# Kernel optimization log

Measured on AMD Instinct MI355X. Metric: run time of the kernel, lower is better.

## Reference

```python
import jax, jax.numpy as jnp
import numpy as np

B, L, G, N, K, E = 64, 512, 128, 32, 8, 65536
NTOK, D_TOK, H_DIR, NTL_INP, NHID, NREL = 10000, 64, 64, 32, 16, 16


def _bn(x, gamma, beta, eps=1e-5):
    # training-mode BatchNorm1d over axis 0; x: (n, C)
    mu = x.mean(0)
    var = x.var(0)
    return gamma * (x - mu) / jnp.sqrt(var + eps) + beta


def _lstm(x, w_ih, w_hh, b_ih, b_hh):
    # x: (B, T, D); torch gate order i, f, g, o
    nb = x.shape[0]
    H = w_hh.shape[1]
    def step(carry, xt):
        h, c = carry
        g = xt @ w_ih.T + b_ih + h @ w_hh.T + b_hh
        i, f, gg, o = jnp.split(g, 4, axis=-1)
        c = jax.nn.sigmoid(f) * c + jax.nn.sigmoid(i) * jnp.tanh(gg)
        h = jax.nn.sigmoid(o) * jnp.tanh(c)
        return (h, c), h
    init = (jnp.zeros((nb, H), x.dtype), jnp.zeros((nb, H), x.dtype))
    _, hs = jax.lax.scan(step, init, jnp.swapaxes(x, 0, 1))
    return jnp.swapaxes(hs, 0, 1)


def setup_inputs() -> dict:
    key = jax.random.key(0)
    ks = jax.random.split(key, 24)
    inp = {}
    inp['seq'] = jax.random.randint(ks[0], (B, L), 0, NTOK)
    inp['pos2grp'] = jax.random.randint(ks[1], (B, L), 0, G)
    inp['idx'] = jax.random.randint(ks[2], (B, N, K), 0, L)
    inp['u'] = jax.random.randint(ks[3], (E,), 0, B * N)
    inp['v'] = jax.random.randint(ks[4], (E,), 0, B * N)
    # parameters
    s = 1.0 / np.sqrt(H_DIR)
    inp['tok_emb'] = jax.random.normal(ks[5], (NTOK, D_TOK), jnp.float32)
    for tag, k0 in (('f', 6), ('b', 10)):
        inp[f'w_ih_{tag}'] = s * jax.random.normal(ks[k0], (4 * H_DIR, D_TOK), jnp.float32)
        inp[f'w_hh_{tag}'] = s * jax.random.normal(ks[k0 + 1], (4 * H_DIR, H_DIR), jnp.float32)
        inp[f'b_ih_{tag}'] = s * jax.random.normal(ks[k0 + 2], (4 * H_DIR,), jnp.float32)
        inp[f'b_hh_{tag}'] = s * jax.random.normal(ks[k0 + 3], (4 * H_DIR,), jnp.float32)
    inp['w_src'] = (1.0 / np.sqrt(2 * H_DIR)) * jax.random.normal(ks[14], (NTL_INP, 2 * H_DIR), jnp.float32)
    inp['b_src'] = jnp.zeros((NTL_INP,), jnp.float32)
    inp['w_dst'] = (1.0 / np.sqrt(2 * H_DIR)) * jax.random.normal(ks[15], (NTL_INP, 2 * H_DIR), jnp.float32)
    inp['b_dst'] = jnp.zeros((NTL_INP,), jnp.float32)
    inp['g_src'] = jnp.ones((NTL_INP,), jnp.float32)
    inp['be_src'] = jnp.zeros((NTL_INP,), jnp.float32)
    inp['g_dst'] = jnp.ones((NTL_INP,), jnp.float32)
    inp['be_dst'] = jnp.zeros((NTL_INP,), jnp.float32)
    inp['ntl_w'] = 0.001 * jax.random.normal(ks[16], (NREL, NHID, NTL_INP, NTL_INP), jnp.float32)
    inp['ntl_v'] = 0.001 * jax.random.normal(ks[17], (NREL, NHID, 2 * NTL_INP), jnp.float32)
    inp['ntl_b'] = jnp.zeros((NREL, NHID, 1), jnp.float32)
    inp['ntl_u'] = 0.001 * jax.random.normal(ks[18], (NREL, 1, NHID), jnp.float32)
    inp['ntl_g'] = jnp.ones((NREL * NHID,), jnp.float32)
    inp['ntl_be'] = jnp.zeros((NREL * NHID,), jnp.float32)
    return inp


def reference(seq, pos2grp, idx, u, v, tok_emb,
              w_ih_f, w_hh_f, b_ih_f, b_hh_f,
              w_ih_b, w_hh_b, b_ih_b, b_hh_b,
              w_src, b_src, w_dst, b_dst,
              g_src, be_src, g_dst, be_dst,
              ntl_w, ntl_v, ntl_b, ntl_u, ntl_g, ntl_be):
    # token embed + scatter-sum tokens -> groups
    x_tok = tok_emb[seq]                                   # (B, L, D)
    gid = (pos2grp + jnp.arange(B)[:, None] * G).reshape(-1)
    x_grp = jax.ops.segment_sum(x_tok.reshape(B * L, -1), gid,
                                num_segments=B * G).reshape(B, G, -1)
    # bidirectional LSTM over groups
    hf = _lstm(x_grp, w_ih_f, w_hh_f, b_ih_f, b_hh_f)
    hb = jnp.flip(_lstm(jnp.flip(x_grp, 1), w_ih_b, w_hh_b, b_ih_b, b_hh_b), 1)
    h_grp = jnp.concatenate([hf, hb], -1)                  # (B, G, 2H)
    # hierarchical gather + sum: node <- sum over K token positions' groups
    b_idx = jnp.arange(B)[:, None, None]
    g_idx = pos2grp[b_idx, idx]                            # (B, N, K)
    h = h_grp[b_idx, g_idx].sum(2).reshape(B * N, -1)      # (B*N, 2H)
    # edge endpoint projections + batchnorm
    hs = _bn(h[u] @ w_src.T + b_src, g_src, be_src)        # (E, ninp)
    ht = _bn(h[v] @ w_dst.T + b_dst, g_dst, be_dst)
    # Neural Tensor Layer
    linear = jnp.einsum('rhd,nd->rhn', ntl_v, jnp.concatenate([hs, ht], 1))
    bil = jnp.stack([
        jnp.einsum('nhj,nj->hn', jnp.einsum('ni,hij->nhj', hs, ntl_w[r]), ht)
        for r in range(NREL)], 0)                          # (R, H, E)
    z = bil + linear + ntl_b
    mu = z.mean(-1, keepdims=True)
    var = z.var(-1, keepdims=True)
    zn = ntl_g.reshape(NREL, NHID, 1) * (z - mu) / jnp.sqrt(var + 1e-5) \
         + ntl_be.reshape(NREL, NHID, 1)
    t = jnp.tanh(zn)
    logit = jnp.einsum('rh,rhn->nr', ntl_u[:, 0, :], t)    # (E, R)
    return logit
```

## Files before the change

kernel.cpp:

```cpp
#include <hip/hip_runtime.h>
#include <hip/hip_bf16.h>
#include <hip/hip_fp16.h>
#include <cstdint>

constexpr int B_   = 64;
constexpr int L_   = 512;
constexpr int G_   = 128;
constexpr int E_   = 65536;
constexpr int RH   = 256;
constexpr int M_   = 2048;
constexpr int JA   = 33;
constexpr int COLS = RH * JA;
constexpr int NREP = 16;

typedef _Float16 v2h __attribute__((ext_vector_type(2)));
typedef _Float16 v8h __attribute__((ext_vector_type(8)));
typedef float    v4f __attribute__((ext_vector_type(4)));
typedef union { uint4 u4; v8h h8; } cvt8;

#define DEV static __device__ __forceinline__

DEV float sigm(float x) { return 1.f / (1.f + __expf(-x)); }
DEV float tanh_fast(float x) {
    x = fminf(15.f, fmaxf(-15.f, x));
    float e = __expf(2.f * x);
    return (e - 1.f) / (e + 1.f);
}

__global__ __launch_bounds__(256) void k_eh(const int* __restrict__ seq,
                                            const int* __restrict__ p2g,
                                            const float* __restrict__ emb,
                                            const int* __restrict__ u,
                                            const int* __restrict__ v,
                                            const float* __restrict__ ntlw,
                                            const float* __restrict__ ntlv,
                                            const float* __restrict__ ntlb,
                                            float* __restrict__ xg,
                                            int* __restrict__ cu, int* __restrict__ cv,
                                            float* __restrict__ waug) {
    int blk = blockIdx.x;
    int t   = threadIdx.x;
    if (blk >= 320) {
        int gid = (blk - 320) * 256 + t;
        int i   = gid / COLS;
        int rem = gid - i * COLS;
        int rh  = rem / JA;
        int j   = rem - rh * JA;
        float val;
        if (i < 32) val = (j < 32) ? ntlw[((size_t)rh * 32 + i) * 32 + j] : ntlv[rh * 64 + i];
        else        val = (j < 32) ? ntlv[rh * 64 + 32 + j] : ntlb[rh];
        waug[(size_t)i * COLS + j * 256 + rh] = val;
        return;
    }
    if (blk >= 64) {
        int n = (blk - 64) * 256 + t;
        atomicAdd(&cu[u[n]], 1);
        atomicAdd(&cv[v[n]], 1);
        return;
    }
    __shared__ float xgl[G_ * 64];
    for (int i = t; i < G_ * 64; i += 256) xgl[i] = 0.f;
    __syncthreads();
    int b = blk;
    int d = t & 63, part = t >> 6;
#pragma unroll 8
    for (int l = part; l < L_; l += 4) {
        int s = seq[b * L_ + l];
        int g = p2g[b * L_ + l];
        atomicAdd(&xgl[g * 64 + d], emb[s * 64 + d]);
    }
    __syncthreads();
    for (int i = t; i < G_ * 64; i += 256) xg[(size_t)b * G_ * 64 + i] = xgl[i];
}

__global__ __launch_bounds__(256) void k_pre(const float* __restrict__ xg,
                                             const float* __restrict__ wihf,
                                             const float* __restrict__ bihf,
                                             const float* __restrict__ bhhf,
                                             const float* __restrict__ wihb,
                                             const float* __restrict__ bihb,
                                             const float* __restrict__ bhhb,
                                             float* __restrict__ pre,
                                             const int* __restrict__ cu,
                                             int* __restrict__ ustart,
                                             int* __restrict__ ucursor) {
    int blk = blockIdx.x;
    int t   = threadIdx.x;
    if (blk == 512) {
        __shared__ int ps[256];
        int base = t * 8, run = 0;
        int c[8], loc[8];
#pragma unroll
        for (int i = 0; i < 8; i++) c[i] = cu[base + i];
#pragma unroll
        for (int i = 0; i < 8; i++) { loc[i] = run; run += c[i]; }
        ps[t] = run;
        __syncthreads();
        for (int off = 1; off < 256; off <<= 1) {
            int a = (t >= off) ? ps[t - off] : 0;
            __syncthreads();
            ps[t] += a;
            __syncthreads();
        }
        int ex = ps[t] - run;
#pragma unroll
        for (int i = 0; i < 8; i++) { ustart[base + i] = ex + loc[i]; ucursor[base + i] = ex + loc[i]; }
        if (t == 255) ustart[2048] = E_;
        return;
    }
    int dir = blk >> 8;
    const float* wih = dir ? wihb : wihf;
    float bias = dir ? (bihb[t] + bhhb[t]) : (bihf[t] + bhhf[t]);
    int r0 = (blk & 255) * 32;

    float4 wv[16];
#pragma unroll
    for (int c = 0; c < 16; c++) wv[c] = ((const float4*)(wih + t * 64))[c];

#pragma unroll 2
    for (int ml = 0; ml < 32; ml++) {
        const float* xr = xg + (size_t)(r0 + ml) * 64;
        float acc = bias;
#pragma unroll
        for (int c = 0; c < 16; c++) {
            float x0 = xr[4 * c], x1 = xr[4 * c + 1], x2 = xr[4 * c + 2], x3 = xr[4 * c + 3];
            acc += x0 * wv[c].x + x1 * wv[c].y + x2 * wv[c].z + x3 * wv[c].w;
        }
        pre[((size_t)dir * 8192 + r0 + ml) * 256 + t] = acc;
    }
}

template <int HALF>
__global__ __launch_bounds__(256, 1) void k_lstm_h(const float* __restrict__ pre,
                                                   const float* __restrict__ whh_f,
                                                   const float* __restrict__ whh_b,
                                                   float* __restrict__ hgrp,
                                                   float* __restrict__ hstate,
                                                   float* __restrict__ cstate,
                                                   const int* __restrict__ u,
                                                   const int* __restrict__ v,
                                                   int* __restrict__ ucursor,
                                                   int2* __restrict__ eonv) {
    int blk = blockIdx.x;
    int t   = threadIdx.x;
    if (HALF == 0 && blk >= 128) {
        int n = (blk - 128) * 256 + t;
        int pos = atomicAdd(&ucursor[u[n]], 1);
        eonv[pos] = make_int2(n, v[n]);
        return;
    }
    __shared__ __align__(16) float plds[64][256];
    __shared__ __align__(16) float hist[64][64];
    __shared__ float gl[2][256];
    int dir = blk >> 6;
    int b   = blk & 63;
    const float* whh = dir ? whh_b : whh_f;
    const float* src = pre + ((size_t)dir * 8192 + (size_t)b * G_) * 256;
    int e = t & 63;
    int q = t >> 6;

    float4 wv[16];
#pragma unroll
    for (int c = 0; c < 16; c++) wv[c] = ((const float4*)(whh + (size_t)t * 64))[c];

    float h, creg;
    if (HALF == 0) { h = 0.f; creg = 0.f; }
    else           { h = hstate[blk * 64 + e]; creg = cstate[blk * 64 + e]; }

    {
        int base = (dir ^ HALF) ? 64 : 0;
        const float4* s4 = (const float4*)(src + (size_t)base * 256);
        float4* d4 = (float4*)&plds[0][0];
#pragma unroll
        for (int i = 0; i < 16; i++) d4[i * 256 + t] = s4[i * 256 + t];
    }
    __syncthreads();
    for (int kk = 0; kk < 64; kk++) {
        int srow = dir ? (63 - kk) : kk;
        float p = plds[srow][t];
        float a0 = p, a1 = 0.f, a2 = 0.f, a3 = 0.f;
#pragma unroll
        for (int c = 0; c < 16; c++) {
            float f0 = __int_as_float(__builtin_amdgcn_readlane(__float_as_int(h), 4 * c + 0));
            float f1 = __int_as_float(__builtin_amdgcn_readlane(__float_as_int(h), 4 * c + 1));
            float f2 = __int_as_float(__builtin_amdgcn_readlane(__float_as_int(h), 4 * c + 2));
            float f3 = __int_as_float(__builtin_amdgcn_readlane(__float_as_int(h), 4 * c + 3));
            a0 += wv[c].x * f0;
            a1 += wv[c].y * f1;
            a2 += wv[c].z * f2;
            a3 += wv[c].w * f3;
        }
        float g = (a0 + a1) + (a2 + a3);
        gl[kk & 1][t] = (q == 2) ? tanh_fast(g) : sigm(g);
        __syncthreads();
        float ai = gl[kk & 1][e];
        float af = gl[kk & 1][64 + e];
        float ag = gl[kk & 1][128 + e];
        float ao = gl[kk & 1][192 + e];
        creg = af * creg + ai * ag;
        h = ao * tanh_fast(creg);
        if (q == 0) hist[srow][e] = h;
    }
    __syncthreads();
    int sbase = (dir ? (1 - HALF) : HALF) * 64;
#pragma unroll
    for (int i = 0; i < 16; i++) {
        int row = q * 16 + i;
        int s = sbase + row;
        hgrp[((size_t)(b * G_ + s)) * 128 + dir * 64 + e] = hist[row][e];
    }
    if (HALF == 0 && q == 0) {
        hstate[blk * 64 + e] = h;
        cstate[blk * 64 + e] = creg;
    }
}

__global__ __launch_bounds__(256) void k_gp(const int* __restrict__ idx,
                                            const int* __restrict__ p2g,
                                            const float* __restrict__ hgrp,
                                            const int* __restrict__ cu,
                                            const int* __restrict__ cv,
                                            const float* __restrict__ wsrc,
                                            const float* __restrict__ bsrc,
                                            const float* __restrict__ wdst,
                                            const float* __restrict__ bdst,
                                            float* __restrict__ Ps, float* __restrict__ Pd,
                                            float* __restrict__ bn_raw) {
    __shared__ __align__(16) float hsl[8][128];
    __shared__ float red[256];
    int m0 = blockIdx.x * 8;
    int t  = threadIdx.x;
    int d = t & 127, mh = t >> 7;
#pragma unroll
    for (int rep = 0; rep < 4; rep++) {
        int ml = rep * 2 + mh;
        int m  = m0 + ml;
        int b  = m >> 5;
        float acc = 0.f;
#pragma unroll
        for (int k = 0; k < 8; k++) {
            int l = idx[m * 8 + k];
            int g = p2g[b * L_ + l];
            acc += hgrp[((size_t)b * G_ + g) * 128 + d];
        }
        hsl[ml][d] = acc;
    }
    __syncthreads();
    int ml = t >> 5, o = t & 31;
    int m  = m0 + ml;
    const float4* hp = (const float4*)&hsl[ml][0];
    float cw_u = (float)cu[m], cw_v = (float)cv[m];
#pragma unroll 1
    for (int side = 0; side < 2; side++) {
        const float* W = side ? wdst : wsrc;
        float4 wr[32];
#pragma unroll
        for (int c = 0; c < 32; c++) wr[c] = ((const float4*)(W + (size_t)o * 128))[c];
        float acc = side ? bdst[o] : bsrc[o];
#pragma unroll
        for (int c = 0; c < 32; c++) {
            float4 h4 = hp[c];
            acc += h4.x * wr[c].x + h4.y * wr[c].y + h4.z * wr[c].z + h4.w * wr[c].w;
        }
        (side ? Pd : Ps)[(size_t)m * 32 + o] = acc;
        float cw = side ? cw_v : cw_u;
        red[t] = cw * acc;
        __syncthreads();
        if (t < 32) {
            float s = 0.f;
#pragma unroll
            for (int i = 0; i < 8; i++) s += red[i * 32 + t];
            atomicAdd(&bn_raw[side * 64 + t], s);
        }
        __syncthreads();
        red[t] = cw * acc * acc;
        __syncthreads();
        if (t < 32) {
            float s = 0.f;
#pragma unroll
            for (int i = 0; i < 8; i++) s += red[i * 32 + t];
            atomicAdd(&bn_raw[side * 64 + 32 + t], s);
        }
        __syncthreads();
    }
}

__global__ __launch_bounds__(256) void k_prep(const float* __restrict__ Ps,
                                              const float* __restrict__ Pd,
                                              const float* __restrict__ bn_raw,
                                              const float* __restrict__ gs,
                                              const float* __restrict__ bes,
                                              const float* __restrict__ gd,
                                              const float* __restrict__ bed,
                                              float* __restrict__ hsaugT,
                                              v2h* __restrict__ htp) {
    int blk = blockIdx.x;
    int t   = threadIdx.x;
    constexpr float invE = 1.f / (float)E_;
    if (blk < 264) {
        int gid = blk * 256 + t;
        int c = gid >> 11;
        int m = gid & 2047;
        float val = 1.f;
        if (c < 32) {
            float mu  = bn_raw[c] * invE;
            float isd = rsqrtf(bn_raw[32 + c] * invE - mu * mu + 1e-5f);
            val = gs[c] * (Ps[(size_t)m * 32 + c] - mu) * isd + bes[c];
        }
        hsaugT[(size_t)c * 2048 + m] = val;
        return;
    }
    int gid = (blk - 264) * 256 + t;
    int m  = gid >> 4;
    int jp = gid & 15;
    int j0 = 2 * jp, j1 = 2 * jp + 1;
    float mu0  = bn_raw[64 + j0] * invE;
    float isd0 = rsqrtf(bn_raw[96 + j0] * invE - mu0 * mu0 + 1e-5f);
    float mu1  = bn_raw[64 + j1] * invE;
    float isd1 = rsqrtf(bn_raw[96 + j1] * invE - mu1 * mu1 + 1e-5f);
    float h0 = gd[j0] * (Pd[(size_t)m * 32 + j0] - mu0) * isd0 + bed[j0];
    float h1 = gd[j1] * (Pd[(size_t)m * 32 + j1] - mu1) * isd1 + bed[j1];
    v2h p;
    p.x = (_Float16)h0; p.y = (_Float16)h1;
    htp[gid] = p;
}

__global__ __launch_bounds__(256) void k_agemm(const float* __restrict__ hsaugT,
                                               const float* __restrict__ waug,
                                               v2h* __restrict__ Ah,
                                               float* __restrict__ A32) {
    int mt = blockIdx.x;
    int jp = blockIdx.y;
    int t  = threadIdx.x;
    if (jp < 16) {
        float w0[JA], w1[JA];
#pragma unroll
        for (int i = 0; i < JA; i++) {
            w0[i] = waug[(size_t)i * COLS + (2 * jp) * 256 + t];
            w1[i] = waug[(size_t)i * COLS + (2 * jp + 1) * 256 + t];
        }
        float acc0[32], acc1[32];
#pragma unroll
        for (int ml = 0; ml < 32; ml++) { acc0[ml] = 0.f; acc1[ml] = 0.f; }
#pragma unroll 3
        for (int i = 0; i < JA; i++) {
            const float* hr = hsaugT + (size_t)i * 2048 + mt * 32;
#pragma unroll
            for (int ml = 0; ml < 32; ml++) {
                acc0[ml] += hr[ml] * w0[i];
                acc1[ml] += hr[ml] * w1[i];
            }
        }
#pragma unroll
        for (int ml = 0; ml < 32; ml++) {
            v2h p;
            p.x = (_Float16)acc0[ml]; p.y = (_Float16)acc1[ml];
            Ah[(size_t)(mt * 32 + ml) * 4096 + jp * 256 + t] = p;
        }
    } else {
        float w2[JA];
#pragma unroll
        for (int i = 0; i < JA; i++) w2[i] = waug[(size_t)i * COLS + 32 * 256 + t];
        float acc[32];
#pragma unroll
        for (int ml = 0; ml < 32; ml++) acc[ml] = 0.f;
#pragma unroll 3
        for (int i = 0; i < JA; i++) {
            const float* hr = hsaugT + (size_t)i * 2048 + mt * 32;
#pragma unroll
            for (int ml = 0; ml < 32; ml++) acc[ml] += hr[ml] * w2[i];
        }
#pragma unroll
        for (int ml = 0; ml < 32; ml++)
            A32[(size_t)(mt * 32 + ml) * 256 + t] = acc[ml];
    }
}

__global__ __launch_bounds__(256) void k_z(const unsigned int* __restrict__ Ah,
                                           const float* __restrict__ A32,
                                           const uint4* __restrict__ htp4,
                                           const int* __restrict__ ustart,
                                           const int2* __restrict__ eonv,
                                           _Float16* __restrict__ zh,
                                           float* __restrict__ zsumR,
                                           float* __restrict__ zsqR) {
    int t    = threadIdx.x;
    int lane = t & 63;
    int uu   = blockIdx.x * 4 + (t >> 6);
    int l15  = lane & 15, quad = lane >> 4;

    uint4 bf[16];
#pragma unroll
    for (int nt = 0; nt < 16; nt++) {
        const unsigned int* bp = Ah + (size_t)uu * 4096 + (quad * 4) * 256 + nt * 16 + l15;
        bf[nt].x = bp[0]; bf[nt].y = bp[256]; bf[nt].z = bp[512]; bf[nt].w = bp[768];
    }
    float a32[16];
#pragma unroll
    for (int nt = 0; nt < 16; nt++) a32[nt] = A32[(size_t)uu * 256 + nt * 16 + l15];

    float s1[16], s2[16];
#pragma unroll
    for (int nt = 0; nt < 16; nt++) { s1[nt] = 0.f; s2[nt] = 0.f; }

    int e0 = ustart[uu], e1 = ustart[uu + 1];
    for (int base = e0; base < e1; base += 16) {
        int ei = min(base + l15, e1 - 1);
        int2 q = eonv[ei];
        uint4 afu = htp4[(size_t)q.y * 4 + quad];
        cvt8 ac; ac.u4 = afu;
        int nrow[4], valid[4];
#pragma unroll
        for (int r = 0; r < 4; r++) {
            int er = quad * 4 + r;
            nrow[r]  = __builtin_amdgcn_ds_bpermute(er << 2, q.x);
            valid[r] = (base + er) < e1;
        }
#pragma unroll
        for (int nt = 0; nt < 16; nt++) {
            cvt8 bc; bc.u4 = bf[nt];
            v4f acc = { a32[nt], a32[nt], a32[nt], a32[nt] };
            acc = __builtin_amdgcn_mfma_f32_16x16x32_f16(ac.h8, bc.h8, acc, 0, 0, 0);
#pragma unroll
            for (int r = 0; r < 4; r++) {
                if (valid[r]) {
                    float z = acc[r];
                    zh[(size_t)nrow[r] * 256 + nt * 16 + l15] = (_Float16)z;
                    s1[nt] += z; s2[nt] += z * z;
                }
            }
        }
    }
    int rep = (blockIdx.x & (NREP - 1)) * 256;
#pragma unroll
    for (int nt = 0; nt < 16; nt++) {
        float a = s1[nt], b = s2[nt];
        a += __shfl_xor(a, 16); a += __shfl_xor(a, 32);
        b += __shfl_xor(b, 16); b += __shfl_xor(b, 32);
        if (quad == 0) {
            atomicAdd(&zsumR[rep + nt * 16 + l15], a);
            atomicAdd(&zsqR[rep + nt * 16 + l15], b);
        }
    }
}

__global__ __launch_bounds__(256) void k_logit(const _Float16* __restrict__ zh,
                                               const float* __restrict__ zsumR,
                                               const float* __restrict__ zsqR,
                                               const float* __restrict__ ntlu,
                                               const float* __restrict__ ntlg,
                                               const float* __restrict__ ntlbe,
                                               float* __restrict__ out) {
    int t  = threadIdx.x;
    int n0 = blockIdx.x * 16;
    float su = 0.f, sq = 0.f;
#pragma unroll
    for (int r = 0; r < NREP; r++) {
        su += zsumR[r * 256 + t];
        sq += zsqR[r * 256 + t];
    }
    float mu  = su / (float)E_;
    float var = sq / (float)E_ - mu * mu;
    float isd = rsqrtf(var + 1e-5f);
    float g   = ntlg[t],  be  = ntlbe[t];
    float uw  = ntlu[t];
    float zv[16];
#pragma unroll
    for (int nl = 0; nl < 16; nl++)
        zv[nl] = (float)zh[(size_t)(n0 + nl) * 256 + t];
#pragma unroll 1
    for (int nl = 0; nl < 16; nl++) {
        float zn  = g * (zv[nl] - mu) * isd + be;
        float val = uw * tanh_fast(zn);
        val += __shfl_xor(val, 1);
        val += __shfl_xor(val, 2);
        val += __shfl_xor(val, 4);
        val += __shfl_xor(val, 8);
        if ((t & 15) == 0) out[(size_t)(n0 + nl) * 16 + (t >> 4)] = val;
    }
}

extern "C" void kernel_launch(void* const* d_in, const int* in_sizes, int n_in,
                              void* d_out, int out_size, void* d_ws, size_t ws_size,
                              hipStream_t stream) {
    const int*   seq   = (const int*)d_in[0];
    const int*   p2g   = (const int*)d_in[1];
    const int*   idx   = (const int*)d_in[2];
    const int*   u     = (const int*)d_in[3];
    const int*   v     = (const int*)d_in[4];
    const float* emb   = (const float*)d_in[5];
    const float* wihf  = (const float*)d_in[6];
    const float* whhf  = (const float*)d_in[7];
    const float* bihf  = (const float*)d_in[8];
    const float* bhhf  = (const float*)d_in[9];
    const float* wihb  = (const float*)d_in[10];
    const float* whhb  = (const float*)d_in[11];
    const float* bihb  = (const float*)d_in[12];
    const float* bhhb  = (const float*)d_in[13];
    const float* wsrc  = (const float*)d_in[14];
    const float* bsrc  = (const float*)d_in[15];
    const float* wdst  = (const float*)d_in[16];
    const float* bdst  = (const float*)d_in[17];
    const float* gs    = (const float*)d_in[18];
    const float* bes   = (const float*)d_in[19];
    const float* gd    = (const float*)d_in[20];
    const float* bed   = (const float*)d_in[21];
    const float* ntlw  = (const float*)d_in[22];
    const float* ntlv  = (const float*)d_in[23];
    const float* ntlb  = (const float*)d_in[24];
    const float* ntlu  = (const float*)d_in[25];
    const float* ntlg  = (const float*)d_in[26];
    const float* ntlbe = (const float*)d_in[27];
    float* out = (float*)d_out;

    char* ws = (char*)d_ws;
    size_t off = 0;
    auto take = [&](size_t bytes) -> char* {
        char* p = ws + off;
        off = (off + bytes + 255) & ~(size_t)255;
        return p;
    };
    int*   cnt_u  = (int*)  take(2048 * 4);
    int*   cnt_v  = (int*)  take(2048 * 4);
    float* zsumR  = (float*)take((size_t)NREP * 256 * 4);
    float* zsqR   = (float*)take((size_t)NREP * 256 * 4);
    float* bn_raw = (float*)take(128 * 4);
    size_t zero_bytes = off;
    float* x_grp   = (float*)take((size_t)B_ * G_ * 64 * 4);
    int*   ucursor = (int*)  take(2048 * 4);
    int*   ustart  = (int*)  take(2049 * 4);
    int2*  eonv    = (int2*) take((size_t)E_ * 8);
    float* pre     = (float*)take((size_t)2 * 8192 * 256 * 4);
    float* hgrp    = (float*)take((size_t)B_ * G_ * 128 * 4);
    float* hstate  = (float*)take((size_t)128 * 64 * 4);
    float* cstate  = (float*)take((size_t)128 * 64 * 4);
    float* Psrc    = (float*)take((size_t)M_ * 32 * 4);
    float* Pdst    = (float*)take((size_t)M_ * 32 * 4);
    float* hsaugT  = (float*)take((size_t)36 * 2048 * 4);
    v2h*   htp     = (v2h*)  take((size_t)M_ * 16 * 4);
    float* waug    = (float*)take((size_t)JA * COLS * 4);
    v2h*   Ah      = (v2h*)  take((size_t)M_ * 4096 * 4);
    float* A32     = (float*)take((size_t)M_ * 256 * 4);
    _Float16* zbuf = (_Float16*)take((size_t)E_ * 256 * 2);
    (void)ws_size; (void)in_sizes; (void)n_in; (void)out_size;

    hipMemsetAsync(d_ws, 0, zero_bytes, stream);

    k_eh<<<320 + 1089, 256, 0, stream>>>(seq, p2g, emb, u, v, ntlw, ntlv, ntlb,
                                         x_grp, cnt_u, cnt_v, waug);
    k_pre<<<513, 256, 0, stream>>>(x_grp, wihf, bihf, bhhf, wihb, bihb, bhhb, pre,
                                   cnt_u, ustart, ucursor);
    k_lstm_h<0><<<384, 256, 0, stream>>>(pre, whhf, whhb, hgrp, hstate, cstate,
                                         u, v, ucursor, eonv);
    k_lstm_h<1><<<128, 256, 0, stream>>>(pre, whhf, whhb, hgrp, hstate, cstate,
                                         u, v, ucursor, eonv);
    k_gp<<<M_ / 8, 256, 0, stream>>>(idx, p2g, hgrp, cnt_u, cnt_v,
                                     wsrc, bsrc, wdst, bdst, Psrc, Pdst, bn_raw);
    k_prep<<<392, 256, 0, stream>>>(Psrc, Pdst, bn_raw, gs, bes, gd, bed, hsaugT, htp);
    k_agemm<<<dim3(64, 17), 256, 0, stream>>>(hsaugT, waug, Ah, A32);
    k_z<<<512, 256, 0, stream>>>((const unsigned int*)Ah, A32, (const uint4*)htp,
                                 ustart, eonv, zbuf, zsumR, zsqR);
    k_logit<<<E_ / 16, 256, 0, stream>>>(zbuf, zsumR, zsqR, ntlu, ntlg, ntlbe, out);
}
```

Before: 375.1 us.

## Split embedding scatter across blocks, merge LSTM halves, shrink agemm tile

The group-embedding scatter now uses four blocks per batch, each covering 128 positions with indices staged in LDS, and the partial sums are merged into a zeroed global buffer with atomics. The two half-sequence LSTM launches become one kernel that runs all 128 steps, which removes the h/c state round trip and one launch. The A-GEMM row tile drops from 32 to 8 rows, giving four times as many blocks. These changes trade more global atomics, a longer serial LSTM block and less weight reuse per block for more parallelism in the scatter and GEMM.

```diff
diff --git a/kernel.cpp b/kernel.cpp
--- a/kernel.cpp
+++ b/kernel.cpp
@@ -40,8 +40,8 @@
                                             float* __restrict__ waug) {
     int blk = blockIdx.x;
     int t   = threadIdx.x;
-    if (blk >= 320) {
-        int gid = (blk - 320) * 256 + t;
+    if (blk >= 512) {
+        int gid = (blk - 512) * 256 + t;
         int i   = gid / COLS;
         int rem = gid - i * COLS;
         int rh  = rem / JA;
@@ -52,25 +52,37 @@
         waug[(size_t)i * COLS + j * 256 + rh] = val;
         return;
     }
-    if (blk >= 64) {
-        int n = (blk - 64) * 256 + t;
+    if (blk >= 256) {
+        int n = (blk - 256) * 256 + t;
         atomicAdd(&cu[u[n]], 1);
         atomicAdd(&cv[v[n]], 1);
         return;
     }
     __shared__ float xgl[G_ * 64];
+    __shared__ int sl[128], gld[128];
+    int b = blk >> 2, part = blk & 3;
     for (int i = t; i < G_ * 64; i += 256) xgl[i] = 0.f;
+    if (t < 128) {
+        sl[t]  = seq[b * L_ + part * 128 + t];
+        gld[t] = p2g[b * L_ + part * 128 + t];
+    }
     __syncthreads();
-    int b = blk;
-    int d = t & 63, part = t >> 6;
-#pragma unroll 8
-    for (int l = part; l < L_; l += 4) {
-        int s = seq[b * L_ + l];
-        int g = p2g[b * L_ + l];
-        atomicAdd(&xgl[g * 64 + d], emb[s * 64 + d]);
+    int d = t & 63, sub = t >> 6;
+#pragma unroll
+    for (int gg = 0; gg < 2; gg++) {
+        int sv[16], gv[16];
+#pragma unroll
+        for (int k = 0; k < 16; k++) {
+            sv[k] = sl[sub * 32 + gg * 16 + k];
+            gv[k] = gld[sub * 32 + gg * 16 + k];
+        }
+#pragma unroll
+        for (int k = 0; k < 16; k++)
+            atomicAdd(&xgl[gv[k] * 64 + d], emb[(size_t)sv[k] * 64 + d]);
     }
     __syncthreads();
-    for (int i = t; i < G_ * 64; i += 256) xg[(size_t)b * G_ * 64 + i] = xgl[i];
+    for (int i = t; i < G_ * 64; i += 256)
+        atomicAdd(&xg[(size_t)b * G_ * 64 + i], xgl[i]);
 }
 
 __global__ __launch_bounds__(256) void k_pre(const float* __restrict__ xg,
@@ -130,20 +142,17 @@
     }
 }
 
-template <int HALF>
-__global__ __launch_bounds__(256, 1) void k_lstm_h(const float* __restrict__ pre,
-                                                   const float* __restrict__ whh_f,
-                                                   const float* __restrict__ whh_b,
-                                                   float* __restrict__ hgrp,
-                                                   float* __restrict__ hstate,
-                                                   float* __restrict__ cstate,
-                                                   const int* __restrict__ u,
-                                                   const int* __restrict__ v,
-                                                   int* __restrict__ ucursor,
-                                                   int2* __restrict__ eonv) {
+__global__ __launch_bounds__(256, 1) void k_lstm(const float* __restrict__ pre,
+                                                 const float* __restrict__ whh_f,
+                                                 const float* __restrict__ whh_b,
+                                                 float* __restrict__ hgrp,
+                                                 const int* __restrict__ u,
+                                                 const int* __restrict__ v,
+                                                 int* __restrict__ ucursor,
+                                                 int2* __restrict__ eonv) {
     int blk = blockIdx.x;
     int t   = threadIdx.x;
-    if (HALF == 0 && blk >= 128) {
+    if (blk >= 128) {
         int n = (blk - 128) * 256 + t;
         int pos = atomicAdd(&ucursor[u[n]], 1);
         eonv[pos] = make_int2(n, v[n]);
@@ -163,55 +172,52 @@
 #pragma unroll
     for (int c = 0; c < 16; c++) wv[c] = ((const float4*)(whh + (size_t)t * 64))[c];
 
-    float h, creg;
-    if (HALF == 0) { h = 0.f; creg = 0.f; }
-    else           { h = hstate[blk * 64 + e]; creg = cstate[blk * 64 + e]; }
-
-    {
-        int base = (dir ^ HALF) ? 64 : 0;
-        const float4* s4 = (const float4*)(src + (size_t)base * 256);
-        float4* d4 = (float4*)&plds[0][0];
-#pragma unroll
-        for (int i = 0; i < 16; i++) d4[i * 256 + t] = s4[i * 256 + t];
-    }
-    __syncthreads();
-    for (int kk = 0; kk < 64; kk++) {
-        int srow = dir ? (63 - kk) : kk;
-        float p = plds[srow][t];
-        float a0 = p, a1 = 0.f, a2 = 0.f, a3 = 0.f;
-#pragma unroll
-        for (int c = 0; c < 16; c++) {
-            float f0 = __int_as_float(__builtin_amdgcn_readlane(__float_as_int(h), 4 * c + 0));
-            float f1 = __int_as_float(__builtin_amdgcn_readlane(__float_as_int(h), 4 * c + 1));
-            float f2 = __int_as_float(__builtin_amdgcn_readlane(__float_as_int(h), 4 * c + 2));
-            float f3 = __int_as_float(__builtin_amdgcn_readlane(__float_as_int(h), 4 * c + 3));
-            a0 += wv[c].x * f0;
-            a1 += wv[c].y * f1;
-            a2 += wv[c].z * f2;
-            a3 += wv[c].w * f3;
-        }
-        float g = (a0 + a1) + (a2 + a3);
-        gl[kk & 1][t] = (q == 2) ? tanh_fast(g) : sigm(g);
-        __syncthreads();
-        float ai = gl[kk & 1][e];
-        float af = gl[kk & 1][64 + e];
-        float ag = gl[kk & 1][128 + e];
-        float ao = gl[kk & 1][192 + e];
-        creg = af * creg + ai * ag;
-        h = ao * tanh_fast(creg);
-        if (q == 0) hist[srow][e] = h;
-    }
-    __syncthreads();
-    int sbase = (dir ? (1 - HALF) : HALF) * 64;
-#pragma unroll
-    for (int i = 0; i < 16; i++) {
-        int row = q * 16 + i;
-        int s = sbase + row;
-        hgrp[((size_t)(b * G_ + s)) * 128 + dir * 64 + e] = hist[row][e];
-    }
-    if (HALF == 0 && q == 0) {
-        hstate[blk * 64 + e] = h;
-        cstate[blk * 64 + e] = creg;
+    float h = 0.f, creg = 0.f;
+
+    for (int half = 0; half < 2; half++) {
+        {
+            int base = (dir ^ half) ? 64 : 0;
+            const float4* s4 = (const float4*)(src + (size_t)base * 256);
+            float4* d4 = (float4*)&plds[0][0];
+#pragma unroll
+            for (int i = 0; i < 16; i++) d4[i * 256 + t] = s4[i * 256 + t];
+        }
+        __syncthreads();
+        for (int kk = 0; kk < 64; kk++) {
+            int k = half * 64 + kk;
+            int srow = dir ? (63 - kk) : kk;
+            float p = plds[srow][t];
+            float a0 = p, a1 = 0.f, a2 = 0.f, a3 = 0.f;
+#pragma unroll
+            for (int c = 0; c < 16; c++) {
+                float f0 = __int_as_float(__builtin_amdgcn_readlane(__float_as_int(h), 4 * c + 0));
+                float f1 = __int_as_float(__builtin_amdgcn_readlane(__float_as_int(h), 4 * c + 1));
+                float f2 = __int_as_float(__builtin_amdgcn_readlane(__float_as_int(h), 4 * c + 2));
+                float f3 = __int_as_float(__builtin_amdgcn_readlane(__float_as_int(h), 4 * c + 3));
+                a0 += wv[c].x * f0;
+                a1 += wv[c].y * f1;
+                a2 += wv[c].z * f2;
+                a3 += wv[c].w * f3;
+            }
+            float g = (a0 + a1) + (a2 + a3);
+            gl[k & 1][t] = (q == 2) ? tanh_fast(g) : sigm(g);
+            __syncthreads();
+            float ai = gl[k & 1][e];
+            float af = gl[k & 1][64 + e];
+            float ag = gl[k & 1][128 + e];
+            float ao = gl[k & 1][192 + e];
+            creg = af * creg + ai * ag;
+            h = ao * tanh_fast(creg);
+            if (q == 0) hist[srow][e] = h;
+        }
+        __syncthreads();
+        int sbase = (dir ? (1 - half) : half) * 64;
+#pragma unroll
+        for (int i = 0; i < 16; i++) {
+            int row = q * 16 + i;
+            int s = sbase + row;
+            hgrp[((size_t)(b * G_ + s)) * 128 + dir * 64 + e] = hist[row][e];
+        }
     }
 }
 
@@ -339,40 +345,40 @@
             w0[i] = waug[(size_t)i * COLS + (2 * jp) * 256 + t];
             w1[i] = waug[(size_t)i * COLS + (2 * jp + 1) * 256 + t];
         }
-        float acc0[32], acc1[32];
-#pragma unroll
-        for (int ml = 0; ml < 32; ml++) { acc0[ml] = 0.f; acc1[ml] = 0.f; }
+        float acc0[8], acc1[8];
+#pragma unroll
+        for (int ml = 0; ml < 8; ml++) { acc0[ml] = 0.f; acc1[ml] = 0.f; }
 #pragma unroll 3
         for (int i = 0; i < JA; i++) {
-            const float* hr = hsaugT + (size_t)i * 2048 + mt * 32;
-#pragma unroll
-            for (int ml = 0; ml < 32; ml++) {
+            const float* hr = hsaugT + (size_t)i * 2048 + mt * 8;
+#pragma unroll
+            for (int ml = 0; ml < 8; ml++) {
                 acc0[ml] += hr[ml] * w0[i];
                 acc1[ml] += hr[ml] * w1[i];
             }
         }
 #pragma unroll
-        for (int ml = 0; ml < 32; ml++) {
+        for (int ml = 0; ml < 8; ml++) {
             v2h p;
             p.x = (_Float16)acc0[ml]; p.y = (_Float16)acc1[ml];
-            Ah[(size_t)(mt * 32 + ml) * 4096 + jp * 256 + t] = p;
+            Ah[(size_t)(mt * 8 + ml) * 4096 + jp * 256 + t] = p;
         }
     } else {
         float w2[JA];
 #pragma unroll
         for (int i = 0; i < JA; i++) w2[i] = waug[(size_t)i * COLS + 32 * 256 + t];
-        float acc[32];
-#pragma unroll
-        for (int ml = 0; ml < 32; ml++) acc[ml] = 0.f;
+        float acc[8];
+#pragma unroll
+        for (int ml = 0; ml < 8; ml++) acc[ml] = 0.f;
 #pragma unroll 3
         for (int i = 0; i < JA; i++) {
-            const float* hr = hsaugT + (size_t)i * 2048 + mt * 32;
-#pragma unroll
-            for (int ml = 0; ml < 32; ml++) acc[ml] += hr[ml] * w2[i];
-        }
-#pragma unroll
-        for (int ml = 0; ml < 32; ml++)
-            A32[(size_t)(mt * 32 + ml) * 256 + t] = acc[ml];
+            const float* hr = hsaugT + (size_t)i * 2048 + mt * 8;
+#pragma unroll
+            for (int ml = 0; ml < 8; ml++) acc[ml] += hr[ml] * w2[i];
+        }
+#pragma unroll
+        for (int ml = 0; ml < 8; ml++)
+            A32[(size_t)(mt * 8 + ml) * 256 + t] = acc[ml];
     }
 }
 
@@ -525,15 +531,13 @@
     float* zsumR  = (float*)take((size_t)NREP * 256 * 4);
     float* zsqR   = (float*)take((size_t)NREP * 256 * 4);
     float* bn_raw = (float*)take(128 * 4);
+    float* x_grp  = (float*)take((size_t)B_ * G_ * 64 * 4);
     size_t zero_bytes = off;
-    float* x_grp   = (float*)take((size_t)B_ * G_ * 64 * 4);
     int*   ucursor = (int*)  take(2048 * 4);
     int*   ustart  = (int*)  take(2049 * 4);
     int2*  eonv    = (int2*) take((size_t)E_ * 8);
     float* pre     = (float*)take((size_t)2 * 8192 * 256 * 4);
     float* hgrp    = (float*)take((size_t)B_ * G_ * 128 * 4);
-    float* hstate  = (float*)take((size_t)128 * 64 * 4);
-    float* cstate  = (float*)take((size_t)128 * 64 * 4);
     float* Psrc    = (float*)take((size_t)M_ * 32 * 4);
     float* Pdst    = (float*)take((size_t)M_ * 32 * 4);
     float* hsaugT  = (float*)take((size_t)36 * 2048 * 4);
@@ -546,18 +550,15 @@
 
     hipMemsetAsync(d_ws, 0, zero_bytes, stream);
 
-    k_eh<<<320 + 1089, 256, 0, stream>>>(seq, p2g, emb, u, v, ntlw, ntlv, ntlb,
+    k_eh<<<512 + 1089, 256, 0, stream>>>(seq, p2g, emb, u, v, ntlw, ntlv, ntlb,
                                          x_grp, cnt_u, cnt_v, waug);
     k_pre<<<513, 256, 0, stream>>>(x_grp, wihf, bihf, bhhf, wihb, bihb, bhhb, pre,
                                    cnt_u, ustart, ucursor);
-    k_lstm_h<0><<<384, 256, 0, stream>>>(pre, whhf, whhb, hgrp, hstate, cstate,
-                                         u, v, ucursor, eonv);
-    k_lstm_h<1><<<128, 256, 0, stream>>>(pre, whhf, whhb, hgrp, hstate, cstate,
-                                         u, v, ucursor, eonv);
+    k_lstm<<<384, 256, 0, stream>>>(pre, whhf, whhb, hgrp, u, v, ucursor, eonv);
     k_gp<<<M_ / 8, 256, 0, stream>>>(idx, p2g, hgrp, cnt_u, cnt_v,
                                      wsrc, bsrc, wdst, bdst, Psrc, Pdst, bn_raw);
     k_prep<<<392, 256, 0, stream>>>(Psrc, Pdst, bn_raw, gs, bes, gd, bed, hsaugT, htp);
-    k_agemm<<<dim3(64, 17), 256, 0, stream>>>(hsaugT, waug, Ah, A32);
+    k_agemm<<<dim3(256, 17), 256, 0, stream>>>(hsaugT, waug, Ah, A32);
     k_z<<<512, 256, 0, stream>>>((const unsigned int*)Ah, A32, (const uint4*)htp,
                                  ustart, eonv, zbuf, zsumR, zsqR);
     k_logit<<<E_ / 16, 256, 0, stream>>>(zbuf, zsumR, zsqR, ntlu, ntlg, ntlbe, out);
```

New measurement: 406.6 us. 1.08x slower.
